# Kernel optimization log

Measured on AMD Instinct MI355X. Metric: run time of the kernel, lower is better.

The kernel has to match this reference:

```python
import jax, jax.numpy as jnp
import numpy as np

B, C, S, D = 4, 16, 512, 512
H = 8
HD = D // H
FFN = 2048
MAX_WL = 10000.0
ROPE_PCT = 0.5
EPS = 1e-5


def setup_inputs() -> dict:
    key = jax.random.key(0)
    ks = jax.random.split(key, 8)
    w = lambda k, shape: jax.random.normal(k, shape, jnp.float32) * 0.02
    return {
        "x": jax.random.normal(ks[0], (B, C, S, D), jnp.float32),
        "Wq": w(ks[1], (D, D)), "bq": jnp.zeros((D,), jnp.float32),
        "Wk": w(ks[2], (D, D)), "bk": jnp.zeros((D,), jnp.float32),
        "Wv": w(ks[3], (D, D)), "bv": jnp.zeros((D,), jnp.float32),
        "Wo": w(ks[4], (D, D)), "bo": jnp.zeros((D,), jnp.float32),
        "ln1_g": jnp.ones((D,), jnp.float32), "ln1_b": jnp.zeros((D,), jnp.float32),
        "ln3_g": jnp.ones((D,), jnp.float32), "ln3_b": jnp.zeros((D,), jnp.float32),
        "W1": w(ks[5], (D, FFN)), "b1": jnp.zeros((FFN,), jnp.float32),
        "W2": w(ks[6], (FFN, D)), "b2": jnp.zeros((D,), jnp.float32),
    }


def _layernorm(x, g, b):
    mu = jnp.mean(x, axis=-1, keepdims=True)
    var = jnp.mean((x - mu) ** 2, axis=-1, keepdims=True)
    return (x - mu) * jax.lax.rsqrt(var + EPS) * g + b


def _p_rope(x, pos):
    # partial rotary: rotate first ROPE_PCT fraction of rotation angles, pass rest through
    half = HD // 2
    rope_angles = int(ROPE_PCT * HD) // 2  # 16 for HD=64, pct=0.5
    exps = (2.0 / HD) * jnp.arange(rope_angles, dtype=jnp.float32)
    timescale = MAX_WL ** exps
    timescale = jnp.concatenate([timescale, jnp.full((half - rope_angles,), jnp.inf, jnp.float32)])
    ang = pos[:, None] / timescale[None, :]  # (S, half); inf timescale -> angle 0 -> identity
    sin, cos = jnp.sin(ang), jnp.cos(ang)
    x1, x2 = x[..., :half], x[..., half:]
    return jnp.concatenate([x1 * cos - x2 * sin, x2 * cos + x1 * sin], axis=-1)


def _forward(x, Wq, bq, Wk, bk, Wv, bv, Wo, bo, ln1_g, ln1_b, ln3_g, ln3_b, W1, b1, W2, b2):
    h = x.reshape(B * C, S, D)
    # --- temporal self-attention (pre-norm) ---
    hn = _layernorm(h, ln1_g, ln1_b)
    scaling = HD ** -0.5
    q = (hn @ Wq + bq) * scaling
    k = hn @ Wk + bk
    v = hn @ Wv + bv
    split = lambda t: t.reshape(B * C, S, H, HD).transpose(0, 2, 1, 3)  # (BC,H,S,HD)
    q, k, v = split(q), split(k), split(v)
    pos = jnp.arange(S, dtype=jnp.float32)
    q = _p_rope(q, pos)
    k = _p_rope(k, pos)
    attn = jax.nn.softmax(jnp.einsum('bhqd,bhkd->bhqk', q, k), axis=-1)
    o = jnp.einsum('bhqk,bhkd->bhqd', attn, v)
    o = o.transpose(0, 2, 1, 3).reshape(B * C, S, D) @ Wo + bo
    h = h + o
    # --- feed-forward (pre-norm) ---
    hn = _layernorm(h, ln3_g, ln3_b)
    ff = jax.nn.gelu(hn @ W1 + b1, approximate=False) @ W2 + b2
    h = h + ff
    return h.reshape(B, C, S, D)


def reference(x, Wq, bq, Wk, bk, Wv, bv, Wo, bo, ln1_g, ln1_b, ln3_g, ln3_b, W1, b1, W2, b2):
    return _forward(x, Wq, bq, Wk, bk, Wv, bv, Wo, bo, ln1_g, ln1_b, ln3_g, ln3_b, W1, b1, W2, b2)
```

## Files before the change

kernel.cpp:

```cpp
#include <hip/hip_runtime.h>
#include <math.h>

typedef unsigned short u16;
typedef __attribute__((ext_vector_type(8))) short bf16x8;
typedef __attribute__((ext_vector_type(4))) float f32x4;

#define MFMA16(a, b, c) __builtin_amdgcn_mfma_f32_16x16x32_bf16((a), (b), (c), 0, 0, 0)

__device__ __forceinline__ u16 f2bf(float f) {
    union { float f; unsigned u; } v; v.f = f;
    unsigned u = v.u;
    unsigned r = (u + 0x7FFFu + ((u >> 16) & 1u)) >> 16;
    return (u16)r;
}

__device__ __forceinline__ unsigned pack_bf16(float lo, float hi) {
    union { float f; unsigned u; } a, b; a.f = lo; b.f = hi;
    return __builtin_amdgcn_perm(b.u + 0x8000u, a.u + 0x8000u, 0x07060302u);
}

__device__ __forceinline__ float fexp2(float x) {
#if __has_builtin(__builtin_amdgcn_exp2f)
    return __builtin_amdgcn_exp2f(x);
#else
    return __expf(x * 0.6931471805599453f);
#endif
}

__device__ __forceinline__ float frcp(float x) {
#if __has_builtin(__builtin_amdgcn_rcpf)
    return __builtin_amdgcn_rcpf(x);
#else
    return 1.0f / x;
#endif
}

__device__ __forceinline__ float fgelu(float v) {
    float x2 = v * v;
    float u = v * (0.7978845608028654f + 0.035677408136300125f * x2);
    return v * frcp(1.0f + fexp2(-2.8853900817779268f * u));
}

__device__ __forceinline__ void gl_lds16(const u16* g, u16* l) {
    __builtin_amdgcn_global_load_lds(
        (const __attribute__((address_space(1))) unsigned*)g,
        (__attribute__((address_space(3))) unsigned*)l, 16, 0, 0);
}

__global__ __launch_bounds__(256) void transpose_cvt_all(
    const float* __restrict__ Wq, const float* __restrict__ Wk,
    const float* __restrict__ Wv, const float* __restrict__ Wo,
    const float* __restrict__ W1, const float* __restrict__ W2,
    u16* __restrict__ wqt, u16* __restrict__ wkt, u16* __restrict__ wvt,
    u16* __restrict__ wot, u16* __restrict__ w1t, u16* __restrict__ w2t)
{
    __shared__ float tile[64][65];
    int fb = blockIdx.x;
    const float* src; u16* dst; int K, N, bx, by;
    if (fb < 256) {
        int w = fb >> 6, b = fb & 63;
        src = (w == 0) ? Wq : (w == 1) ? Wk : (w == 2) ? Wv : Wo;
        dst = (w == 0) ? wqt : (w == 1) ? wkt : (w == 2) ? wvt : wot;
        K = 512; N = 512; bx = b & 7; by = b >> 3;
    } else if (fb < 512) {
        int b = fb - 256; src = W1; dst = w1t; K = 512; N = 2048; bx = b & 31; by = b >> 5;
    } else {
        int b = fb - 512; src = W2; dst = w2t; K = 2048; N = 512; bx = b & 7; by = b >> 3;
    }
    int n0 = bx * 64, k0 = by * 64;
    int tx = threadIdx.x & 63, ty = threadIdx.x >> 6;
    #pragma unroll
    for (int i = ty; i < 64; i += 4)
        tile[i][tx] = src[(size_t)(k0 + i) * N + n0 + tx];
    __syncthreads();
    #pragma unroll
    for (int i = ty; i < 64; i += 4)
        dst[(size_t)(n0 + i) * K + k0 + tx] = f2bf(tile[tx][i]);
}

__global__ __launch_bounds__(256) void ln_kernel(const float* __restrict__ in,
                                                 u16* __restrict__ out,
                                                 const float* __restrict__ g,
                                                 const float* __restrict__ b) {
    int row = blockIdx.x;
    const float* rp = in + (size_t)row * 512;
    int t = threadIdx.x;
    float2 v = *(const float2*)(rp + t * 2);
    float s = v.x + v.y;
    float sq = v.x * v.x + v.y * v.y;
    #pragma unroll
    for (int off = 32; off > 0; off >>= 1) {
        s  += __shfl_down(s, off, 64);
        sq += __shfl_down(sq, off, 64);
    }
    __shared__ float red[8];
    __shared__ float stat[2];
    int wid = t >> 6;
    if ((t & 63) == 0) { red[wid] = s; red[wid + 4] = sq; }
    __syncthreads();
    if (t == 0) {
        float S = red[0] + red[1] + red[2] + red[3];
        float Q = red[4] + red[5] + red[6] + red[7];
        float mu = S * (1.0f / 512.0f);
        float var = Q * (1.0f / 512.0f) - mu * mu;
        stat[0] = mu;
        stat[1] = rsqrtf(var + 1e-5f);
    }
    __syncthreads();
    float mu = stat[0], inv = stat[1];
    int c = t * 2;
    float2 gv = *(const float2*)(g + c);
    float2 bv = *(const float2*)(b + c);
    ushort2 ov;
    ov.x = f2bf((v.x - mu) * inv * gv.x + bv.x);
    ov.y = f2bf((v.y - mu) * inv * gv.y + bv.y);
    *(ushort2*)(out + (size_t)row * 512 + c) = ov;
}


#define FENCE() asm volatile("" ::: "memory")
#define BARF()  do { FENCE(); __builtin_amdgcn_s_barrier(); FENCE(); } while (0)
#define LGKM0() asm volatile("s_waitcnt lgkmcnt(0)" ::: "memory")
#define VM4()   asm volatile("s_waitcnt vmcnt(4)" ::: "memory")
#define VM0()   asm volatile("s_waitcnt vmcnt(0)" ::: "memory")
#define PRIO1() __builtin_amdgcn_s_setprio(1)
#define PRIO0() __builtin_amdgcn_s_setprio(0)

__device__ __forceinline__ bf16x8 ldfrag(const u16* __restrict__ base, int R, int ko, int lq) {
    int o = (ko + lq * 8) ^ ((R & 7) * 8);
    return *(const bf16x8*)(base + R * 64 + o);
}

__device__ __forceinline__ void gemm256_core(
    const u16* __restrict__ A, const u16* __restrict__ Bt, int K,
    int m0, int n0, int t, u16* __restrict__ smem, f32x4 (&acc)[8][4])
{
    const int NS = K >> 6;
    const int wid = t >> 6, lane = t & 63;
    const int lm = lane & 15, lq = lane >> 4;
    const int wm_ = wid >> 2;
    const int wn_ = wid & 3;
    const int wbh = wn_ >> 1;
    const int wbr = (wn_ & 1) * 64;

    auto reg = [&](int buf, int ab, int half) -> u16* {
        return smem + (((buf << 1) | ab) * 2 + half) * 8192;
    };

    const int r0 = t >> 3;
    const int csw = ((t & 7) * 8) ^ ((r0 & 7) * 8);
    const u16* gA = A + (size_t)(m0 + r0) * K + csw;
    const u16* gB = Bt + (size_t)(n0 + r0) * K + csw;
    const size_t pK64 = (size_t)64 * K;
    const size_t hK128 = (size_t)128 * K;

    auto stA = [&](int u, int hf) {
        if (u >= NS) return;
        u16* d = reg(u & 1, 0, hf) + t * 8;
        const u16* s = gA + (size_t)(u * 64) + (hf ? hK128 : (size_t)0);
        gl_lds16(s, d);
        gl_lds16(s + pK64, d + 4096);
    };
    auto stB = [&](int u, int hf) {
        if (u >= NS) return;
        u16* d = reg(u & 1, 1, hf) + t * 8;
        const u16* s = gB + (size_t)(u * 64) + (hf ? hK128 : (size_t)0);
        gl_lds16(s, d);
        gl_lds16(s + pK64, d + 4096);
    };

    #pragma unroll
    for (int i = 0; i < 8; ++i)
        #pragma unroll
        for (int j = 0; j < 4; ++j) acc[i][j] = (f32x4){0.f, 0.f, 0.f, 0.f};

    stB(0, 0); stB(0, 1); stA(0, 0); stA(0, 1);
    stB(1, 0); stB(1, 1);
    VM4();
    BARF();

    for (int s = 0; s < NS; ++s) {
        const u16* As = reg(s & 1, 0, wm_);
        const u16* Bs = reg(s & 1, 1, wbh);
        bf16x8 aF[4], bF[4][2];
        #pragma unroll
        for (int i = 0; i < 4; ++i) aF[i] = ldfrag(As, i * 16 + lm, 0, lq);
        #pragma unroll
        for (int j = 0; j < 4; ++j) bF[j][0] = ldfrag(Bs, wbr + j * 16 + lm, 0, lq);
        stA(s + 1, 0);
        stA(s + 1, 1);
        BARF(); PRIO1();
        #pragma unroll
        for (int i = 0; i < 4; ++i)
            #pragma unroll
            for (int j = 0; j < 4; ++j)
                acc[i][j] = MFMA16(aF[i], bF[j][0], acc[i][j]);
        PRIO0(); LGKM0(); BARF();
        #pragma unroll
        for (int i = 0; i < 4; ++i) aF[i] = ldfrag(As, i * 16 + lm, 32, lq);
        #pragma unroll
        for (int j = 0; j < 4; ++j) bF[j][1] = ldfrag(Bs, wbr + j * 16 + lm, 32, lq);
        BARF(); PRIO1();
        #pragma unroll
        for (int i = 0; i < 4; ++i)
            #pragma unroll
            for (int j = 0; j < 4; ++j)
                acc[i][j] = MFMA16(aF[i], bF[j][1], acc[i][j]);
        PRIO0(); LGKM0(); BARF();
        #pragma unroll
        for (int i = 0; i < 4; ++i) aF[i] = ldfrag(As, 64 + i * 16 + lm, 0, lq);
        stB(s + 2, 0);
        BARF(); PRIO1();
        #pragma unroll
        for (int i = 0; i < 4; ++i)
            #pragma unroll
            for (int j = 0; j < 4; ++j)
                acc[4 + i][j] = MFMA16(aF[i], bF[j][0], acc[4 + i][j]);
        PRIO0(); LGKM0(); BARF();
        #pragma unroll
        for (int i = 0; i < 4; ++i) aF[i] = ldfrag(As, 64 + i * 16 + lm, 32, lq);
        stB(s + 2, 1);
        BARF(); PRIO1();
        #pragma unroll
        for (int i = 0; i < 4; ++i)
            #pragma unroll
            for (int j = 0; j < 4; ++j)
                acc[4 + i][j] = MFMA16(aF[i], bF[j][1], acc[4 + i][j]);
        PRIO0(); LGKM0();
        if (s >= NS - 2) { VM0(); } else { VM4(); }
        BARF();
    }
}

__global__ __launch_bounds__(512) void qkv256_kernel(
    const u16* __restrict__ A,
    const u16* __restrict__ wqt, const u16* __restrict__ wkt, const u16* __restrict__ wvt,
    const float* __restrict__ bqp, const float* __restrict__ bkp, const float* __restrict__ bvp,
    u16* __restrict__ qb, u16* __restrict__ kb, u16* __restrict__ vb, float sclq)
{
    __shared__ u16 smem[65536];
    int flat = blockIdx.x;
    int xcd = flat & 7, slot = flat >> 3;
    int g = xcd * 96 + slot;
    int mt = g / 6, nt = g % 6;
    int mode = nt >> 1;
    int m0 = mt * 256, nb0 = (nt & 1) * 256;
    const u16* Bt = (mode == 0) ? wqt : (mode == 1) ? wkt : wvt;
    const float* bias = (mode == 0) ? bqp : (mode == 1) ? bkp : bvp;
    u16* outp = (mode == 0) ? qb : (mode == 1) ? kb : vb;

    int t = threadIdx.x;
    f32x4 acc[8][4];
    gemm256_core(A, Bt, 512, m0, nb0, t, smem, acc);

    int wid = t >> 6, lane = t & 63, lm = lane & 15, lq = lane >> 4;
    int rowb = m0 + (wid >> 2) * 128;
    int colb = nb0 + (wid & 3) * 64;

    if (mode < 2) {
        float bv0 = bias[colb + 0 * 16 + lm];
        float bv1 = bias[colb + 1 * 16 + lm];
        float bv2 = bias[colb + 2 * 16 + lm];
        float bv3 = bias[colb + 3 * 16 + lm];
        float its = __expf((float)lm * -0.28782313662425572f);
        float scl = (mode == 0) ? sclq : 1.f;
        #pragma unroll
        for (int i = 0; i < 8; ++i) {
            #pragma unroll
            for (int r = 0; r < 4; ++r) {
                int gm = rowb + i * 16 + lq * 4 + r;
                int s = gm & 511;
                float ang = (float)s * its;
                float sn = __sinf(ang), cs = __cosf(ang);
                float x1 = acc[i][0][r] + bv0;
                float x2 = acc[i][2][r] + bv2;
                float y0 = (x1 * cs - x2 * sn) * scl;
                float y2 = (x2 * cs + x1 * sn) * scl;
                float y1 = (acc[i][1][r] + bv1) * scl;
                float y3 = (acc[i][3][r] + bv3) * scl;
                size_t base = ((size_t)(gm >> 9)) * 262144 + (size_t)(colb >> 6) * 32768
                            + (size_t)s * 64 + lm;
                outp[base +  0] = f2bf(y0);
                outp[base + 16] = f2bf(y1);
                outp[base + 32] = f2bf(y2);
                outp[base + 48] = f2bf(y3);
            }
        }
    } else {
        #pragma unroll
        for (int i = 0; i < 8; ++i)
            #pragma unroll
            for (int j = 0; j < 4; ++j) {
                int gn = colb + j * 16 + lm;
                float bvv = bias[gn];
                #pragma unroll
                for (int r = 0; r < 4; ++r) {
                    int gm = rowb + i * 16 + lq * 4 + r;
                    float v = acc[i][j][r] + bvv;
                    size_t idx = ((size_t)(gm >> 9)) * 262144 + (size_t)(gn >> 6) * 32768
                               + (size_t)(gn & 63) * 512 + (gm & 511);
                    outp[idx] = f2bf(v);
                }
            }
    }
}

template<int MODE>
__global__ __launch_bounds__(512) void gemm256_kernel(
    const u16* __restrict__ A, const u16* __restrict__ Bt,
    const float* __restrict__ bias, const float* __restrict__ res,
    void* __restrict__ outp, int M, int N, int K)
{
    __shared__ u16 smem[65536];
    int flat = blockIdx.x;
    int nbt = N >> 8;
    int nwg = (M >> 8) * nbt;
    int xcd = flat & 7, slot = flat >> 3;
    int g = xcd * (nwg >> 3) + slot;
    int mt = g / nbt, nt = g % nbt;
    int m0 = mt * 256, n0 = nt * 256;

    int t = threadIdx.x;
    f32x4 acc[8][4];
    gemm256_core(A, Bt, K, m0, n0, t, smem, acc);

    int wid = t >> 6, lane = t & 63, lm = lane & 15, lq = lane >> 4;
    int rowb = m0 + (wid >> 2) * 128, colb = n0 + (wid & 3) * 64;
    #pragma unroll
    for (int i = 0; i < 8; ++i)
        #pragma unroll
        for (int j = 0; j < 4; ++j) {
            int gn = colb + j * 16 + lm;
            float bv = bias[gn];
            #pragma unroll
            for (int r = 0; r < 4; ++r) {
                int gm = rowb + i * 16 + lq * 4 + r;
                float v = acc[i][j][r] + bv;
                if (MODE == 3) {
                    size_t idx = (size_t)gm * N + gn;
                    ((float*)outp)[idx] = v + res[idx];
                } else {
                    ((u16*)outp)[(size_t)gm * N + gn] = f2bf(fgelu(v));
                }
            }
        }
}

__global__ __launch_bounds__(256) void attn_kernel(
    const u16* __restrict__ q, const u16* __restrict__ k,
    const u16* __restrict__ vt, u16* __restrict__ o)
{
    int flat = blockIdx.y * gridDim.x + blockIdx.x;
    int xcd = flat & 7, slot = flat >> 3;
    int nh = xcd * 64 + (slot >> 1);
    int qt = slot & 1;
    const u16* Qb = q + (size_t)nh * 32768 + (size_t)qt * 16384;
    const u16* Kb = k + (size_t)nh * 32768;
    const u16* Vb = vt + (size_t)nh * 32768;
    __shared__ u16 lK[64][72], lV[64][72];
    __shared__ u16 lP[4][16][72];
    int t = threadIdx.x, wid = t >> 6, lane = t & 63, lm = lane & 15, lq = lane >> 4;

    bf16x8 bq[4][2];
    #pragma unroll
    for (int sub = 0; sub < 4; ++sub) {
        const u16* qr = Qb + (size_t)(sub * 64 + wid * 16 + lm) * 64;
        bq[sub][0] = *(const bf16x8*)(qr + lq * 8);
        bq[sub][1] = *(const bf16x8*)(qr + 32 + lq * 8);
    }

    const f32x4 zero = {0.f, 0.f, 0.f, 0.f};
    f32x4 Oacc[4][4];
    float mo[4], l[4];
    #pragma unroll
    for (int s = 0; s < 4; ++s) {
        mo[s] = -INFINITY; l[s] = 0.f;
        #pragma unroll
        for (int d = 0; d < 4; ++d) Oacc[s][d] = zero;
    }

    for (int kt = 0; kt < 8; ++kt) {
        #pragma unroll
        for (int p = 0; p < 2; ++p) {
            int idx = p * 256 + t, row = idx >> 3, ch = (idx & 7) * 8;
            *(uint4*)&lK[row][ch] = *(const uint4*)(Kb + (size_t)(kt * 64 + row) * 64 + ch);
            *(uint4*)&lV[row][ch] = *(const uint4*)(Vb + (size_t)row * 512 + kt * 64 + ch);
        }
        __syncthreads();
        bf16x8 aK[4][2], aV[4][2];
        #pragma unroll
        for (int i = 0; i < 4; ++i) {
            aK[i][0] = *(const bf16x8*)&lK[i * 16 + lm][lq * 8];
            aK[i][1] = *(const bf16x8*)&lK[i * 16 + lm][32 + lq * 8];
            aV[i][0] = *(const bf16x8*)&lV[i * 16 + lm][lq * 8];
            aV[i][1] = *(const bf16x8*)&lV[i * 16 + lm][32 + lq * 8];
        }
        #pragma unroll
        for (int sub = 0; sub < 4; ++sub) {
            f32x4 sc[4];
            #pragma unroll
            for (int i = 0; i < 4; ++i) {
                f32x4 z = MFMA16(aK[i][0], bq[sub][0], zero);
                sc[i] = MFMA16(aK[i][1], bq[sub][1], z);
            }
            float mx = sc[0][0];
            #pragma unroll
            for (int i = 0; i < 4; ++i)
                #pragma unroll
                for (int r = 0; r < 4; ++r) mx = fmaxf(mx, sc[i][r]);
            mx = fmaxf(mx, __shfl_xor(mx, 16, 64));
            mx = fmaxf(mx, __shfl_xor(mx, 32, 64));
            float mn = fmaxf(mo[sub], mx);
            float al = fexp2(mo[sub] - mn);
            float pv[4][4], sum = 0.f;
            #pragma unroll
            for (int i = 0; i < 4; ++i)
                #pragma unroll
                for (int r = 0; r < 4; ++r) { pv[i][r] = fexp2(sc[i][r] - mn); sum += pv[i][r]; }
            sum += __shfl_xor(sum, 16, 64);
            sum += __shfl_xor(sum, 32, 64);
            l[sub] = l[sub] * al + sum;
            mo[sub] = mn;
            #pragma unroll
            for (int dn = 0; dn < 4; ++dn) Oacc[sub][dn] *= al;
            #pragma unroll
            for (int i = 0; i < 4; ++i) {
                uint2 w2;
                w2.x = pack_bf16(pv[i][0], pv[i][1]);
                w2.y = pack_bf16(pv[i][2], pv[i][3]);
                *(uint2*)&lP[wid][lm][i * 16 + lq * 4] = w2;
            }
            bf16x8 bp0 = *(const bf16x8*)&lP[wid][lm][lq * 8];
            bf16x8 bp1 = *(const bf16x8*)&lP[wid][lm][32 + lq * 8];
            #pragma unroll
            for (int dn = 0; dn < 4; ++dn) {
                Oacc[sub][dn] = MFMA16(aV[dn][0], bp0, Oacc[sub][dn]);
                Oacc[sub][dn] = MFMA16(aV[dn][1], bp1, Oacc[sub][dn]);
            }
        }
        __syncthreads();
    }
    int bc = nh >> 3, h = nh & 7;
    #pragma unroll
    for (int sub = 0; sub < 4; ++sub) {
        float inv = 1.f / l[sub];
        size_t orow = ((size_t)(bc * 512 + qt * 256 + sub * 64 + wid * 16 + lm)) * 512 + h * 64;
        #pragma unroll
        for (int dn = 0; dn < 4; ++dn) {
            uint2 w2;
            w2.x = pack_bf16(Oacc[sub][dn][0] * inv, Oacc[sub][dn][1] * inv);
            w2.y = pack_bf16(Oacc[sub][dn][2] * inv, Oacc[sub][dn][3] * inv);
            *(uint2*)(o + orow + dn * 16 + lq * 4) = w2;
        }
    }
}

extern "C" void kernel_launch(void* const* d_in, const int* in_sizes, int n_in,
                              void* d_out, int out_size, void* d_ws, size_t ws_size,
                              hipStream_t stream) {
    const float* x    = (const float*)d_in[0];
    const float* Wq   = (const float*)d_in[1];
    const float* bq   = (const float*)d_in[2];
    const float* Wk   = (const float*)d_in[3];
    const float* bk   = (const float*)d_in[4];
    const float* Wv   = (const float*)d_in[5];
    const float* bv   = (const float*)d_in[6];
    const float* Wo   = (const float*)d_in[7];
    const float* bo   = (const float*)d_in[8];
    const float* ln1g = (const float*)d_in[9];
    const float* ln1b = (const float*)d_in[10];
    const float* ln3g = (const float*)d_in[11];
    const float* ln3b = (const float*)d_in[12];
    const float* W1   = (const float*)d_in[13];
    const float* b1   = (const float*)d_in[14];
    const float* W2   = (const float*)d_in[15];
    const float* b2   = (const float*)d_in[16];

    char* ws = (char*)d_ws;
    u16*  hn  = (u16*)(ws + 0ull);
    u16*  qb  = (u16*)(ws + 33554432ull);
    u16*  kb  = (u16*)(ws + 67108864ull);
    u16*  vb  = (u16*)(ws + 100663296ull);
    u16*  ob  = (u16*)(ws + 134217728ull);
    u16*  ffa = (u16*)(ws + 33554432ull);
    float* h1 = (float*)(ws + 167772160ull);
    u16*  wqt = (u16*)(ws + 234881024ull);
    u16*  wkt = (u16*)(ws + 235405312ull);
    u16*  wvt = (u16*)(ws + 235929600ull);
    u16*  wot = (u16*)(ws + 236453888ull);
    u16*  w1t = (u16*)(ws + 236978176ull);
    u16*  w2t = (u16*)(ws + 239075328ull);

    dim3 blk(256);
    transpose_cvt_all<<<768, blk, 0, stream>>>(Wq, Wk, Wv, Wo, W1, W2,
                                               wqt, wkt, wvt, wot, w1t, w2t);

    ln_kernel<<<32768, blk, 0, stream>>>(x, hn, ln1g, ln1b);

    qkv256_kernel<<<768, dim3(512), 0, stream>>>(hn, wqt, wkt, wvt, bq, bk, bv,
                                                 qb, kb, vb,
                                                 0.125f * 1.4426950408889634f);

    attn_kernel<<<dim3(2, 512), blk, 0, stream>>>(qb, kb, vb, ob);

    gemm256_kernel<3><<<256, dim3(512), 0, stream>>>(ob, wot, bo, x, h1,
                                                     32768, 512, 512);

    ln_kernel<<<32768, blk, 0, stream>>>(h1, hn, ln3g, ln3b);

    gemm256_kernel<4><<<1024, dim3(512), 0, stream>>>(hn, w1t, b1, nullptr, ffa,
                                                      32768, 2048, 512);
    gemm256_kernel<3><<<256, dim3(512), 0, stream>>>(ffa, w2t, b2, h1,
                                                     (float*)d_out, 32768, 512, 2048);
}
```

Baseline: 583.3 us.

## Double-buffer attention K/V tiles via direct global-to-LDS loads with swizzle and lazy rescale

The attention kernel now prefetches the next K/V tile into a second LDS buffer using direct global-to-LDS loads, with an XOR swizzle in place of padding to avoid bank conflicts. V fragments are read from LDS inside the PV loop rather than held in registers, and launch bounds request 3 blocks per SM to raise occupancy. The online softmax skips rescaling unless the running max grows by more than 8, which cuts exp and multiply work but allows unnormalized values up to 2^8 in bf16 P. The gain depends on hiding load latency; extra LDS reads per sub-tile and the wider bf16 range are the costs.

```diff
diff --git a/kernel.cpp b/kernel.cpp
--- a/kernel.cpp
+++ b/kernel.cpp
@@ -346,7 +346,7 @@
         }
 }
 
-__global__ __launch_bounds__(256) void attn_kernel(
+__global__ __launch_bounds__(256, 3) void attn_kernel(
     const u16* __restrict__ q, const u16* __restrict__ k,
     const u16* __restrict__ vt, u16* __restrict__ o)
 {
@@ -357,9 +357,24 @@
     const u16* Qb = q + (size_t)nh * 32768 + (size_t)qt * 16384;
     const u16* Kb = k + (size_t)nh * 32768;
     const u16* Vb = vt + (size_t)nh * 32768;
-    __shared__ u16 lK[64][72], lV[64][72];
+    __shared__ u16 sKV[2][2][4096];
     __shared__ u16 lP[4][16][72];
     int t = threadIdx.x, wid = t >> 6, lane = t & 63, lm = lane & 15, lq = lane >> 4;
+
+    auto stKV = [&](int kt, int buf) {
+        if (kt >= 8) return;
+        #pragma unroll
+        for (int p = 0; p < 2; ++p) {
+            int idx = p * 256 + t;
+            int row = idx >> 3;
+            int c = ((idx & 7) * 8) ^ ((row & 7) * 8);
+            gl_lds16(Kb + (size_t)(kt * 64 + row) * 64 + c, &sKV[buf][0][idx * 8]);
+            gl_lds16(Vb + (size_t)row * 512 + kt * 64 + c, &sKV[buf][1][idx * 8]);
+        }
+    };
+    auto ldsw = [&](const u16* base, int row, int cu16) -> bf16x8 {
+        return *(const bf16x8*)&base[row * 64 + (cu16 ^ ((row & 7) * 8))];
+    };
 
     bf16x8 bq[4][2];
     #pragma unroll
@@ -379,21 +394,19 @@
         for (int d = 0; d < 4; ++d) Oacc[s][d] = zero;
     }
 
+    stKV(0, 0);
+    VM0(); BARF();
+
     for (int kt = 0; kt < 8; ++kt) {
-        #pragma unroll
-        for (int p = 0; p < 2; ++p) {
-            int idx = p * 256 + t, row = idx >> 3, ch = (idx & 7) * 8;
-            *(uint4*)&lK[row][ch] = *(const uint4*)(Kb + (size_t)(kt * 64 + row) * 64 + ch);
-            *(uint4*)&lV[row][ch] = *(const uint4*)(Vb + (size_t)row * 512 + kt * 64 + ch);
-        }
-        __syncthreads();
-        bf16x8 aK[4][2], aV[4][2];
+        int buf = kt & 1;
+        stKV(kt + 1, buf ^ 1);
+        const u16* Kl = sKV[buf][0];
+        const u16* Vl = sKV[buf][1];
+        bf16x8 aK[4][2];
         #pragma unroll
         for (int i = 0; i < 4; ++i) {
-            aK[i][0] = *(const bf16x8*)&lK[i * 16 + lm][lq * 8];
-            aK[i][1] = *(const bf16x8*)&lK[i * 16 + lm][32 + lq * 8];
-            aV[i][0] = *(const bf16x8*)&lV[i * 16 + lm][lq * 8];
-            aV[i][1] = *(const bf16x8*)&lV[i * 16 + lm][32 + lq * 8];
+            aK[i][0] = ldsw(Kl, i * 16 + lm, lq * 8);
+            aK[i][1] = ldsw(Kl, i * 16 + lm, 32 + lq * 8);
         }
         #pragma unroll
         for (int sub = 0; sub < 4; ++sub) {
@@ -410,35 +423,45 @@
                 for (int r = 0; r < 4; ++r) mx = fmaxf(mx, sc[i][r]);
             mx = fmaxf(mx, __shfl_xor(mx, 16, 64));
             mx = fmaxf(mx, __shfl_xor(mx, 32, 64));
-            float mn = fmaxf(mo[sub], mx);
-            float al = fexp2(mo[sub] - mn);
-            float pv[4][4], sum = 0.f;
+            if (!__all(mx <= mo[sub] + 8.0f)) {
+                float mn = fmaxf(mo[sub], mx);
+                float al = fexp2(mo[sub] - mn);
+                l[sub] *= al;
+                #pragma unroll
+                for (int dn = 0; dn < 4; ++dn) Oacc[sub][dn] *= al;
+                mo[sub] = mn;
+            }
+            float mc = mo[sub];
+            float sum = 0.f;
             #pragma unroll
             for (int i = 0; i < 4; ++i)
                 #pragma unroll
-                for (int r = 0; r < 4; ++r) { pv[i][r] = fexp2(sc[i][r] - mn); sum += pv[i][r]; }
+                for (int r = 0; r < 4; ++r) {
+                    float p = fexp2(sc[i][r] - mc);
+                    sc[i][r] = p;
+                    sum += p;
+                }
             sum += __shfl_xor(sum, 16, 64);
             sum += __shfl_xor(sum, 32, 64);
-            l[sub] = l[sub] * al + sum;
-            mo[sub] = mn;
-            #pragma unroll
-            for (int dn = 0; dn < 4; ++dn) Oacc[sub][dn] *= al;
+            l[sub] += sum;
             #pragma unroll
             for (int i = 0; i < 4; ++i) {
                 uint2 w2;
-                w2.x = pack_bf16(pv[i][0], pv[i][1]);
-                w2.y = pack_bf16(pv[i][2], pv[i][3]);
+                w2.x = pack_bf16(sc[i][0], sc[i][1]);
+                w2.y = pack_bf16(sc[i][2], sc[i][3]);
                 *(uint2*)&lP[wid][lm][i * 16 + lq * 4] = w2;
             }
             bf16x8 bp0 = *(const bf16x8*)&lP[wid][lm][lq * 8];
             bf16x8 bp1 = *(const bf16x8*)&lP[wid][lm][32 + lq * 8];
             #pragma unroll
             for (int dn = 0; dn < 4; ++dn) {
-                Oacc[sub][dn] = MFMA16(aV[dn][0], bp0, Oacc[sub][dn]);
-                Oacc[sub][dn] = MFMA16(aV[dn][1], bp1, Oacc[sub][dn]);
+                bf16x8 v0 = ldsw(Vl, dn * 16 + lm, lq * 8);
+                bf16x8 v1 = ldsw(Vl, dn * 16 + lm, 32 + lq * 8);
+                Oacc[sub][dn] = MFMA16(v0, bp0, Oacc[sub][dn]);
+                Oacc[sub][dn] = MFMA16(v1, bp1, Oacc[sub][dn]);
             }
         }
-        __syncthreads();
+        LGKM0(); VM0(); BARF();
     }
     int bc = nh >> 3, h = nh & 7;
     #pragma unroll
```

New measurement: 548.9 us. 5.9% less time.
